# Optimization experiments

Measured on AMD Instinct MI355X. Metric: run time of the kernel, lower is better.

The kernel has to match this reference:

```python
import jax, jax.numpy as jnp
import numpy as np

DIM = 1024
N_HIDDEN = 64
NUM_HEADS = 16
B, S = 4, 1024
# original torch code: scale = sqrt(n_hidden // num_heads) = sqrt(64 // 16) = 2.0
SCALE = float(np.sqrt(N_HIDDEN // NUM_HEADS))


def setup_inputs() -> dict:
    key = jax.random.key(0)
    ks = jax.random.split(key, 10)
    lim = 1.0 / np.sqrt(DIM)          # nn.Linear default init range
    lim_o = 1.0 / np.sqrt(N_HIDDEN * NUM_HEADS)
    u = lambda k, shape, l: jax.random.uniform(k, shape, jnp.float32, -l, l)
    x = jax.random.normal(ks[0], (B, S, DIM), jnp.float32)
    attn_mask = jax.random.randint(ks[1], (B, S, S), 0, 2).astype(jnp.int32)
    # stacked per-head projection weights: [H, dim, n_hidden]
    Wq = u(ks[2], (NUM_HEADS, DIM, N_HIDDEN), lim)
    bq = u(ks[3], (NUM_HEADS, N_HIDDEN), lim)
    Wk = u(ks[4], (NUM_HEADS, DIM, N_HIDDEN), lim)
    bk = u(ks[5], (NUM_HEADS, N_HIDDEN), lim)
    Wv = u(ks[6], (NUM_HEADS, DIM, N_HIDDEN), lim)
    bv = u(ks[7], (NUM_HEADS, N_HIDDEN), lim)
    Wo = u(ks[8], (NUM_HEADS * N_HIDDEN, DIM), lim_o)
    bo = u(ks[9], (DIM,), lim_o)
    return {"x": x, "attn_mask": attn_mask, "Wq": Wq, "bq": bq,
            "Wk": Wk, "bk": bk, "Wv": Wv, "bv": bv, "Wo": Wo, "bo": bo}


def reference(x, attn_mask, Wq, bq, Wk, bk, Wv, bv, Wo, bo):
    # batched QKV across all heads (replaces the per-head Python loop)
    Q = jnp.einsum('bsd,hde->bhse', x, Wq) + bq[None, :, None, :]
    K = jnp.einsum('bsd,hde->bhse', x, Wk) + bk[None, :, None, :]
    V = jnp.einsum('bsd,hde->bhse', x, Wv) + bv[None, :, None, :]
    scores = jnp.einsum('bhse,bhte->bhst', Q, K) / SCALE
    alpha = jax.nn.softmax(scores, axis=-1)
    # faithful to original: zero out masked entries AFTER softmax, no renorm
    alpha = jnp.where(attn_mask[:, None, :, :] == 0, 0.0, alpha)  # [B,H,S,S]
    out = jnp.einsum('bhst,bhte->bhse', alpha, V)                 # [B,H,S,E]
    # torch.cat over heads on last dim == reshape to [B,S,H*E] in head order
    concat = out.transpose(0, 2, 1, 3).reshape(B, S, NUM_HEADS * N_HIDDEN)
    attn_output = concat @ Wo + bo                                # [B,S,dim]
    return attn_output, alpha
```

## Files before the change

kernel.cpp:

```cpp
#include <hip/hip_runtime.h>
#include <stdint.h>

#define S_LEN 1024
#define DIM   1024
#define NHID  64
#define NHEAD 16
#define NB    4

typedef __bf16 bf16x8 __attribute__((ext_vector_type(8)));
typedef float  f32x4  __attribute__((ext_vector_type(4)));
typedef unsigned short u16;

#if defined(__has_builtin)
#if __has_builtin(__builtin_amdgcn_global_load_lds)
#define HAS_GLD 1
#endif
#endif

#ifdef HAS_GLD
#define GLD16(gsrc, ldst)                                                    \
  __builtin_amdgcn_global_load_lds(                                         \
      (const __attribute__((address_space(1))) unsigned int*)(gsrc),        \
      (__attribute__((address_space(3))) unsigned int*)(ldst), 16, 0, 0)
#endif

__device__ __forceinline__ u16 f2b(float f) {
  unsigned u = __float_as_uint(f);
  u += 0x7FFFu + ((u >> 16) & 1u);
  return (u16)(u >> 16);
}

__device__ __forceinline__ f32x4 mfma16(bf16x8 a, bf16x8 b, f32x4 c) {
  return __builtin_amdgcn_mfma_f32_16x16x32_bf16(a, b, c, 0, 0, 0);
}

__global__ __launch_bounds__(256) void k_cvt_x(const float* __restrict__ x,
                                               u16* __restrict__ xb) {
  int i = blockIdx.x * 256 + threadIdx.x;
  float4 v = ((const float4*)x)[i];
  ushort4 o;
  o.x = f2b(v.x); o.y = f2b(v.y); o.z = f2b(v.z); o.w = f2b(v.w);
  ((ushort4*)xb)[i] = o;
}

__global__ __launch_bounds__(256) void k_maskbits(const int* __restrict__ mask,
                                                  uint32_t* __restrict__ bits) {
  int w = blockIdx.x * 256 + threadIdx.x;
  const int4* mp = (const int4*)mask + (size_t)w * 8;
  uint32_t v = 0;
#pragma unroll
  for (int i = 0; i < 8; ++i) {
    int4 m = mp[i];
    v |= (m.x != 0 ? 1u : 0u) << (i * 4 + 0);
    v |= (m.y != 0 ? 1u : 0u) << (i * 4 + 1);
    v |= (m.z != 0 ? 1u : 0u) << (i * 4 + 2);
    v |= (m.w != 0 ? 1u : 0u) << (i * 4 + 3);
  }
  bits[w] = v;
}

__global__ __launch_bounds__(256) void k_transpose(const float* __restrict__ in,
                                                   u16* __restrict__ out,
                                                   int R, int C) {
  const float* ip = in + (size_t)blockIdx.x * R * C;
  u16* op = out + (size_t)blockIdx.x * R * C;
  __shared__ float tile[32][65];
  int r0 = blockIdx.y * 32, c0 = blockIdx.z * 64;
  int t = threadIdx.x;
  {
    int col = t & 63, rr = t >> 6;
#pragma unroll
    for (int p = 0; p < 8; ++p) {
      int r = p * 4 + rr;
      tile[r][col] = ip[(size_t)(r0 + r) * C + c0 + col];
    }
  }
  __syncthreads();
  {
    int d = t & 31, er = t >> 5;
#pragma unroll
    for (int p = 0; p < 8; ++p) {
      int e = p * 8 + er;
      op[(size_t)(c0 + e) * R + r0 + d] = f2b(tile[d][e]);
    }
  }
}

__global__ __launch_bounds__(256) void k_qkv(const u16* __restrict__ xb,
                                             const u16* __restrict__ Wtb,
                                             const float* __restrict__ bq,
                                             const float* __restrict__ bk,
                                             const float* __restrict__ bv,
                                             u16* __restrict__ Qb,
                                             u16* __restrict__ Kb,
                                             u16* __restrict__ Vtb) {
  __shared__ __align__(16) char lds[32768];
  int t = threadIdx.x, w = t >> 6, lane = t & 63;
  int l15 = lane & 15, l4 = lane >> 4;
  int m0 = blockIdx.x * 128, n0 = blockIdx.y * 128, sel = blockIdx.z;
  const u16* Wh = Wtb + (size_t)sel * (NHEAD * NHID * DIM);
  int wr = w >> 1, wc = w & 1;

  f32x4 acc[4][4];
  const f32x4 fz = {0.f, 0.f, 0.f, 0.f};
#pragma unroll
  for (int i = 0; i < 4; ++i)
#pragma unroll
    for (int j = 0; j < 4; ++j) acc[i][j] = fz;

  for (int kk = 0; kk < 16; ++kk) {
    int k0 = kk * 64;
#ifdef HAS_GLD
#pragma unroll
    for (int c = 0; c < 4; ++c) {
      int idx = c * 256 + t, r = idx >> 3, cb = idx & 7;
      int sc_ = cb ^ (r & 7);
      GLD16(xb + (size_t)(m0 + r) * DIM + k0 + sc_ * 8,
            lds + (c * 256 + w * 64) * 16);
    }
#pragma unroll
    for (int c = 0; c < 4; ++c) {
      int idx = c * 256 + t, r = idx >> 3, cb = idx & 7;
      int sc_ = cb ^ (r & 7);
      GLD16(Wh + (size_t)(n0 + r) * DIM + k0 + sc_ * 8,
            lds + 16384 + (c * 256 + w * 64) * 16);
    }
#else
#pragma unroll
    for (int c = 0; c < 4; ++c) {
      int idx = c * 256 + t, r = idx >> 3, cb = idx & 7;
      int4 v = *(const int4*)(xb + (size_t)(m0 + r) * DIM + k0 + cb * 8);
      *(int4*)(lds + r * 128 + ((cb * 16) ^ ((r & 7) << 4))) = v;
    }
#pragma unroll
    for (int c = 0; c < 4; ++c) {
      int idx = c * 256 + t, r = idx >> 3, cb = idx & 7;
      int4 v = *(const int4*)(Wh + (size_t)(n0 + r) * DIM + k0 + cb * 8);
      *(int4*)(lds + 16384 + r * 128 + ((cb * 16) ^ ((r & 7) << 4))) = v;
    }
#endif
    __syncthreads();
    bf16x8 a[4][2], bb[4][2];
#pragma unroll
    for (int mf = 0; mf < 4; ++mf)
#pragma unroll
      for (int kc = 0; kc < 2; ++kc) {
        int row = wr * 64 + mf * 16 + l15;
        int kb = kc * 64 + l4 * 16;
        a[mf][kc] = *(const bf16x8*)(lds + row * 128 + (kb ^ ((row & 7) << 4)));
      }
#pragma unroll
    for (int nf = 0; nf < 4; ++nf)
#pragma unroll
      for (int kc = 0; kc < 2; ++kc) {
        int row = wc * 64 + nf * 16 + l15;
        int kb = kc * 64 + l4 * 16;
        bb[nf][kc] = *(const bf16x8*)(lds + 16384 + row * 128 + (kb ^ ((row & 7) << 4)));
      }
#pragma unroll
    for (int kc = 0; kc < 2; ++kc)
#pragma unroll
      for (int mf = 0; mf < 4; ++mf)
#pragma unroll
        for (int nf = 0; nf < 4; ++nf)
          acc[mf][nf] = mfma16(a[mf][kc], bb[nf][kc], acc[mf][nf]);
    __syncthreads();
  }

  const float* bias = (sel == 0) ? bq : (sel == 1) ? bk : bv;
  float postScale = (sel == 0) ? 0.5f : 1.0f;
#pragma unroll
  for (int nf = 0; nf < 4; ++nf) {
    int n = n0 + wc * 64 + nf * 16 + l15;
    int h = n >> 6, e = n & 63;
    float bv_ = bias[n];
#pragma unroll
    for (int mf = 0; mf < 4; ++mf) {
      int mrow0 = m0 + wr * 64 + mf * 16 + l4 * 4;
      int b_ = mrow0 >> 10, s0 = mrow0 & 1023;
      if (sel == 2) {
        ushort4 pk;
        pk.x = f2b(acc[mf][nf][0] + bv_);
        pk.y = f2b(acc[mf][nf][1] + bv_);
        pk.z = f2b(acc[mf][nf][2] + bv_);
        pk.w = f2b(acc[mf][nf][3] + bv_);
        *(ushort4*)(Vtb + ((size_t)(b_ * NHEAD + h) * NHID + e) * S_LEN + s0) = pk;
      } else {
        u16* dst = (sel == 0) ? Qb : Kb;
#pragma unroll
        for (int j = 0; j < 4; ++j)
          dst[((size_t)(b_ * NHEAD + h) * S_LEN + s0 + j) * NHID + e] =
              f2b((acc[mf][nf][j] + bv_) * postScale);
      }
    }
  }
}

__global__ __launch_bounds__(256) void k_attn(const u16* __restrict__ Qb,
                                              const u16* __restrict__ Kb,
                                              const u16* __restrict__ Vtb,
                                              const uint32_t* __restrict__ mbitsG,
                                              float* __restrict__ alphaOut,
                                              u16* __restrict__ Ob) {
  __shared__ __align__(16) char smem[33024];
  float* redS = (float*)(smem + 32768);
  int t = threadIdx.x, w = t >> 6, lane = t & 63;
  int l15 = lane & 15, l4 = lane >> 4;
  int q0 = blockIdx.x * 16;
  int bh = blockIdx.y, b = bh >> 4, hh = bh & 15;
  const u16* Qh = Qb + (size_t)bh * S_LEN * NHID;
  const u16* Kh = Kb + (size_t)bh * S_LEN * NHID;
  const u16* Vh = Vtb + (size_t)bh * NHID * S_LEN;
  int kbase = w * 256;

  const uint32_t* mrow = mbitsG + ((size_t)b * S_LEN + q0 + l15) * 32 + w * 8;
  uint4 mw0 = *(const uint4*)(mrow);
  uint4 mw1 = *(const uint4*)(mrow + 4);

  bf16x8 aq[2];
#pragma unroll
  for (int ec = 0; ec < 2; ++ec)
    aq[ec] = *(const bf16x8*)(Qh + (size_t)(q0 + l15) * NHID + ec * 32 + l4 * 8);

  const f32x4 fz = {0.f, 0.f, 0.f, 0.f};

  float s0 = 0.f, s1 = 0.f, s2 = 0.f, s3 = 0.f;
#pragma unroll
  for (int kf = 0; kf < 16; ++kf) {
    int key = kbase + kf * 16 + l15;
    bf16x8 kb0 = *(const bf16x8*)(Kh + (size_t)key * NHID + l4 * 8);
    bf16x8 kb1 = *(const bf16x8*)(Kh + (size_t)key * NHID + 32 + l4 * 8);
    f32x4 sct = fz;
    sct = mfma16(kb0, aq[0], sct);
    sct = mfma16(kb1, aq[1], sct);
    float e0 = __expf(sct[0]);
    float e1 = __expf(sct[1]);
    float e2 = __expf(sct[2]);
    float e3 = __expf(sct[3]);
    s0 += e0; s1 += e1; s2 += e2; s3 += e3;
    uint32_t mword;
    switch (kf >> 1) {
      case 0: mword = mw0.x; break;
      case 1: mword = mw0.y; break;
      case 2: mword = mw0.z; break;
      case 3: mword = mw0.w; break;
      case 4: mword = mw1.x; break;
      case 5: mword = mw1.y; break;
      case 6: mword = mw1.z; break;
      default: mword = mw1.w; break;
    }
    int bbase = ((kf & 1) << 4) + l4 * 4;
    uint32_t am01 = (((mword >> (bbase + 0)) & 1u) ? 0x0000FFFFu : 0u) |
                    (((mword >> (bbase + 1)) & 1u) ? 0xFFFF0000u : 0u);
    uint32_t am23 = (((mword >> (bbase + 2)) & 1u) ? 0x0000FFFFu : 0u) |
                    (((mword >> (bbase + 3)) & 1u) ? 0xFFFF0000u : 0u);
    uint2 pk;
    pk.x = ((uint32_t)f2b(e0) | ((uint32_t)f2b(e1) << 16)) & am01;
    pk.y = ((uint32_t)f2b(e2) | ((uint32_t)f2b(e3) << 16)) & am23;
    *(uint2*)(smem + l15 * 2048 +
              (((kbase + kf * 16 + l4 * 4) * 2) ^ ((l15 & 7) << 4))) = pk;
  }
  float ls = (s0 + s1) + (s2 + s3);
  ls += __shfl_xor(ls, 16);
  ls += __shfl_xor(ls, 32);
  if (lane < 16) redS[w * 16 + l15] = ls;
  __syncthreads();

  float* abW = alphaOut + (size_t)bh * S_LEN * S_LEN;
  f32x4 o[4];
#pragma unroll
  for (int ef = 0; ef < 4; ++ef) o[ef] = fz;

  auto rw = [&](int rr) {
    int r = w * 4 + rr;
    float invr = 1.f / (redS[r] + redS[16 + r] + redS[32 + r] + redS[48 + r]);
    float* dst = abW + (size_t)(q0 + r) * S_LEN;
#pragma unroll
    for (int seg = 0; seg < 4; ++seg) {
      int raw = seg * 512 + lane * 8;
      int boff = raw ^ ((r & 7) << 4);
      uint2 pk = *(const uint2*)(smem + r * 2048 + boff);
      f32x4 av;
      av[0] = __uint_as_float(pk.x << 16) * invr;
      av[1] = __uint_as_float(pk.x & 0xFFFF0000u) * invr;
      av[2] = __uint_as_float(pk.y << 16) * invr;
      av[3] = __uint_as_float(pk.y & 0xFFFF0000u) * invr;
      __builtin_nontemporal_store(av, (f32x4*)(dst + (raw >> 1)));
    }
  };
  auto pvc = [&](int c) {
#pragma unroll
    for (int kc2 = 0; kc2 < 2; ++kc2) {
      bf16x8 pa = *(const bf16x8*)(smem + l15 * 2048 +
          ((((kbase + c * 64 + kc2 * 32) * 2) + l4 * 16) ^ ((l15 & 7) << 4)));
#pragma unroll
      for (int ef = 0; ef < 4; ++ef) {
        int e = ef * 16 + l15;
        bf16x8 vb = *(const bf16x8*)(Vh + (size_t)e * S_LEN + kbase + c * 64 +
                                     kc2 * 32 + l4 * 8);
        o[ef] = mfma16(pa, vb, o[ef]);
      }
    }
  };

  rw(0); pvc(0);
  rw(1); pvc(1);
  rw(2); pvc(2);
  rw(3); pvc(3);

  __syncthreads();
  float* redO = (float*)smem;
#pragma unroll
  for (int ef = 0; ef < 4; ++ef)
#pragma unroll
    for (int j = 0; j < 4; ++j)
      redO[w * 1024 + (l4 * 4 + j) * 64 + ef * 16 + l15] = o[ef][j];
  __syncthreads();
  {
    int e = t & 63, r4 = t >> 6;
#pragma unroll
    for (int p = 0; p < 4; ++p) {
      int r = p * 4 + r4;
      float invr = 1.f / (redS[r] + redS[16 + r] + redS[32 + r] + redS[48 + r]);
      float s4 = redO[r * 64 + e] + redO[1024 + r * 64 + e] +
                 redO[2048 + r * 64 + e] + redO[3072 + r * 64 + e];
      Ob[(size_t)(b * S_LEN + q0 + r) * DIM + hh * NHID + e] = f2b(s4 * invr);
    }
  }
}

__global__ __launch_bounds__(256) void k_oproj(const u16* __restrict__ Ob,
                                               const u16* __restrict__ Wotb,
                                               const float* __restrict__ bo,
                                               float* __restrict__ out) {
  __shared__ __align__(16) char lds[32768];
  int t = threadIdx.x, w = t >> 6, lane = t & 63;
  int l15 = lane & 15, l4 = lane >> 4;
  int m0 = blockIdx.x * 128, n0 = blockIdx.y * 128;
  int wr = w >> 1, wc = w & 1;
  f32x4 acc[4][4];
  const f32x4 fz = {0.f, 0.f, 0.f, 0.f};
#pragma unroll
  for (int i = 0; i < 4; ++i)
#pragma unroll
    for (int j = 0; j < 4; ++j) acc[i][j] = fz;

  for (int kk = 0; kk < 16; ++kk) {
    int k0 = kk * 64;
#ifdef HAS_GLD
#pragma unroll
    for (int c = 0; c < 4; ++c) {
      int idx = c * 256 + t, r = idx >> 3, cb = idx & 7;
      int sc_ = cb ^ (r & 7);
      GLD16(Ob + (size_t)(m0 + r) * DIM + k0 + sc_ * 8,
            lds + (c * 256 + w * 64) * 16);
    }
#pragma unroll
    for (int c = 0; c < 4; ++c) {
      int idx = c * 256 + t, r = idx >> 3, cb = idx & 7;
      int sc_ = cb ^ (r & 7);
      GLD16(Wotb + (size_t)(n0 + r) * DIM + k0 + sc_ * 8,
            lds + 16384 + (c * 256 + w * 64) * 16);
    }
#else
#pragma unroll
    for (int c = 0; c < 4; ++c) {
      int idx = c * 256 + t, r = idx >> 3, cb = idx & 7;
      int4 v = *(const int4*)(Ob + (size_t)(m0 + r) * DIM + k0 + cb * 8);
      *(int4*)(lds + r * 128 + ((cb * 16) ^ ((r & 7) << 4))) = v;
    }
#pragma unroll
    for (int c = 0; c < 4; ++c) {
      int idx = c * 256 + t, r = idx >> 3, cb = idx & 7;
      int4 v = *(const int4*)(Wotb + (size_t)(n0 + r) * DIM + k0 + cb * 8);
      *(int4*)(lds + 16384 + r * 128 + ((cb * 16) ^ ((r & 7) << 4))) = v;
    }
#endif
    __syncthreads();
    bf16x8 a[4][2], bb[4][2];
#pragma unroll
    for (int mf = 0; mf < 4; ++mf)
#pragma unroll
      for (int kc = 0; kc < 2; ++kc) {
        int row = wr * 64 + mf * 16 + l15;
        int kb = kc * 64 + l4 * 16;
        a[mf][kc] = *(const bf16x8*)(lds + row * 128 + (kb ^ ((row & 7) << 4)));
      }
#pragma unroll
    for (int nf = 0; nf < 4; ++nf)
#pragma unroll
      for (int kc = 0; kc < 2; ++kc) {
        int row = wc * 64 + nf * 16 + l15;
        int kb = kc * 64 + l4 * 16;
        bb[nf][kc] = *(const bf16x8*)(lds + 16384 + row * 128 + (kb ^ ((row & 7) << 4)));
      }
#pragma unroll
    for (int kc = 0; kc < 2; ++kc)
#pragma unroll
      for (int mf = 0; mf < 4; ++mf)
#pragma unroll
        for (int nf = 0; nf < 4; ++nf)
          acc[mf][nf] = mfma16(a[mf][kc], bb[nf][kc], acc[mf][nf]);
    __syncthreads();
  }
#pragma unroll
  for (int nf = 0; nf < 4; ++nf) {
    int n = n0 + wc * 64 + nf * 16 + l15;
    float bv_ = bo[n];
#pragma unroll
    for (int mf = 0; mf < 4; ++mf)
#pragma unroll
      for (int j = 0; j < 4; ++j) {
        int m = m0 + wr * 64 + mf * 16 + l4 * 4 + j;
        out[(size_t)m * DIM + n] = acc[mf][nf][j] + bv_;
      }
  }
}

extern "C" void kernel_launch(void* const* d_in, const int* in_sizes, int n_in,
                              void* d_out, int out_size, void* d_ws, size_t ws_size,
                              hipStream_t stream) {
  const float* x    = (const float*)d_in[0];
  const int*   mask = (const int*)d_in[1];
  const float* Wq   = (const float*)d_in[2];
  const float* bq   = (const float*)d_in[3];
  const float* Wk   = (const float*)d_in[4];
  const float* bk   = (const float*)d_in[5];
  const float* Wv   = (const float*)d_in[6];
  const float* bv   = (const float*)d_in[7];
  const float* Wo   = (const float*)d_in[8];
  const float* bo   = (const float*)d_in[9];
  float* out = (float*)d_out;
  float* alphaOut = out + (size_t)NB * S_LEN * DIM;

  char* ws = (char*)d_ws;
  u16* xb    = (u16*)(ws);
  u16* Wtb   = (u16*)(ws + 8388608);
  u16* Wotb  = (u16*)(ws + 14680064);
  u16* Qb    = (u16*)(ws + 16777216);
  u16* Kb    = (u16*)(ws + 25165824);
  u16* Vtb   = (u16*)(ws + 33554432);
  u16* Ob    = (u16*)(ws + 41943040);
  uint32_t* mbits = (uint32_t*)(ws + 50331648);

  k_maskbits<<<512, 256, 0, stream>>>(mask, mbits);
  k_cvt_x<<<4096, 256, 0, stream>>>(x, xb);
  k_transpose<<<dim3(16, 32, 1), 256, 0, stream>>>(Wq, Wtb,           1024, 64);
  k_transpose<<<dim3(16, 32, 1), 256, 0, stream>>>(Wk, Wtb + 1048576, 1024, 64);
  k_transpose<<<dim3(16, 32, 1), 256, 0, stream>>>(Wv, Wtb + 2097152, 1024, 64);
  k_transpose<<<dim3(1, 32, 16), 256, 0, stream>>>(Wo, Wotb,          1024, 1024);
  k_qkv<<<dim3(32, 8, 3), 256, 0, stream>>>(xb, Wtb, bq, bk, bv, Qb, Kb, Vtb);
  k_attn<<<dim3(64, 64), 256, 0, stream>>>(Qb, Kb, Vtb, mbits, alphaOut, Ob);
  k_oproj<<<dim3(32, 8), 256, 0, stream>>>(Ob, Wotb, bo, out);
}
```

Baseline: 221.8 us.

## Persistent attention blocks and split PV by head-dim across waves

```diff
diff --git a/kernel.cpp b/kernel.cpp
--- a/kernel.cpp
+++ b/kernel.cpp
@@ -206,125 +206,113 @@
   float* redS = (float*)(smem + 32768);
   int t = threadIdx.x, w = t >> 6, lane = t & 63;
   int l15 = lane & 15, l4 = lane >> 4;
-  int q0 = blockIdx.x * 16;
-  int bh = blockIdx.y, b = bh >> 4, hh = bh & 15;
-  const u16* Qh = Qb + (size_t)bh * S_LEN * NHID;
-  const u16* Kh = Kb + (size_t)bh * S_LEN * NHID;
-  const u16* Vh = Vtb + (size_t)bh * NHID * S_LEN;
+  const f32x4 fz = {0.f, 0.f, 0.f, 0.f};
   int kbase = w * 256;
 
-  const uint32_t* mrow = mbitsG + ((size_t)b * S_LEN + q0 + l15) * 32 + w * 8;
-  uint4 mw0 = *(const uint4*)(mrow);
-  uint4 mw1 = *(const uint4*)(mrow + 4);
-
-  bf16x8 aq[2];
-#pragma unroll
-  for (int ec = 0; ec < 2; ++ec)
-    aq[ec] = *(const bf16x8*)(Qh + (size_t)(q0 + l15) * NHID + ec * 32 + l4 * 8);
-
-  const f32x4 fz = {0.f, 0.f, 0.f, 0.f};
-
-  float s0 = 0.f, s1 = 0.f, s2 = 0.f, s3 = 0.f;
-#pragma unroll
-  for (int kf = 0; kf < 16; ++kf) {
-    int key = kbase + kf * 16 + l15;
-    bf16x8 kb0 = *(const bf16x8*)(Kh + (size_t)key * NHID + l4 * 8);
-    bf16x8 kb1 = *(const bf16x8*)(Kh + (size_t)key * NHID + 32 + l4 * 8);
-    f32x4 sct = fz;
-    sct = mfma16(kb0, aq[0], sct);
-    sct = mfma16(kb1, aq[1], sct);
-    float e0 = __expf(sct[0]);
-    float e1 = __expf(sct[1]);
-    float e2 = __expf(sct[2]);
-    float e3 = __expf(sct[3]);
-    s0 += e0; s1 += e1; s2 += e2; s3 += e3;
-    uint32_t mword;
-    switch (kf >> 1) {
-      case 0: mword = mw0.x; break;
-      case 1: mword = mw0.y; break;
-      case 2: mword = mw0.z; break;
-      case 3: mword = mw0.w; break;
-      case 4: mword = mw1.x; break;
-      case 5: mword = mw1.y; break;
-      case 6: mword = mw1.z; break;
-      default: mword = mw1.w; break;
-    }
-    int bbase = ((kf & 1) << 4) + l4 * 4;
-    uint32_t am01 = (((mword >> (bbase + 0)) & 1u) ? 0x0000FFFFu : 0u) |
-                    (((mword >> (bbase + 1)) & 1u) ? 0xFFFF0000u : 0u);
-    uint32_t am23 = (((mword >> (bbase + 2)) & 1u) ? 0x0000FFFFu : 0u) |
-                    (((mword >> (bbase + 3)) & 1u) ? 0xFFFF0000u : 0u);
-    uint2 pk;
-    pk.x = ((uint32_t)f2b(e0) | ((uint32_t)f2b(e1) << 16)) & am01;
-    pk.y = ((uint32_t)f2b(e2) | ((uint32_t)f2b(e3) << 16)) & am23;
-    *(uint2*)(smem + l15 * 2048 +
-              (((kbase + kf * 16 + l4 * 4) * 2) ^ ((l15 & 7) << 4))) = pk;
-  }
-  float ls = (s0 + s1) + (s2 + s3);
-  ls += __shfl_xor(ls, 16);
-  ls += __shfl_xor(ls, 32);
-  if (lane < 16) redS[w * 16 + l15] = ls;
-  __syncthreads();
-
-  float* abW = alphaOut + (size_t)bh * S_LEN * S_LEN;
-  f32x4 o[4];
-#pragma unroll
-  for (int ef = 0; ef < 4; ++ef) o[ef] = fz;
-
-  auto rw = [&](int rr) {
-    int r = w * 4 + rr;
-    float invr = 1.f / (redS[r] + redS[16 + r] + redS[32 + r] + redS[48 + r]);
-    float* dst = abW + (size_t)(q0 + r) * S_LEN;
-#pragma unroll
-    for (int seg = 0; seg < 4; ++seg) {
-      int raw = seg * 512 + lane * 8;
-      int boff = raw ^ ((r & 7) << 4);
-      uint2 pk = *(const uint2*)(smem + r * 2048 + boff);
-      f32x4 av;
-      av[0] = __uint_as_float(pk.x << 16) * invr;
-      av[1] = __uint_as_float(pk.x & 0xFFFF0000u) * invr;
-      av[2] = __uint_as_float(pk.y << 16) * invr;
-      av[3] = __uint_as_float(pk.y & 0xFFFF0000u) * invr;
-      __builtin_nontemporal_store(av, (f32x4*)(dst + (raw >> 1)));
-    }
-  };
-  auto pvc = [&](int c) {
-#pragma unroll
-    for (int kc2 = 0; kc2 < 2; ++kc2) {
-      bf16x8 pa = *(const bf16x8*)(smem + l15 * 2048 +
-          ((((kbase + c * 64 + kc2 * 32) * 2) + l4 * 16) ^ ((l15 & 7) << 4)));
-#pragma unroll
-      for (int ef = 0; ef < 4; ++ef) {
-        int e = ef * 16 + l15;
-        bf16x8 vb = *(const bf16x8*)(Vh + (size_t)e * S_LEN + kbase + c * 64 +
-                                     kc2 * 32 + l4 * 8);
-        o[ef] = mfma16(pa, vb, o[ef]);
-      }
-    }
-  };
-
-  rw(0); pvc(0);
-  rw(1); pvc(1);
-  rw(2); pvc(2);
-  rw(3); pvc(3);
-
-  __syncthreads();
-  float* redO = (float*)smem;
-#pragma unroll
-  for (int ef = 0; ef < 4; ++ef)
-#pragma unroll
-    for (int j = 0; j < 4; ++j)
-      redO[w * 1024 + (l4 * 4 + j) * 64 + ef * 16 + l15] = o[ef][j];
-  __syncthreads();
-  {
-    int e = t & 63, r4 = t >> 6;
-#pragma unroll
-    for (int p = 0; p < 4; ++p) {
-      int r = p * 4 + r4;
+  for (int ii = blockIdx.x; ii < 4096; ii += 1024) {
+    int bh = ii >> 6, q0 = (ii & 63) * 16;
+    int b = bh >> 4, hh = bh & 15;
+    const u16* Qh = Qb + (size_t)bh * S_LEN * NHID;
+    const u16* Kh = Kb + (size_t)bh * S_LEN * NHID;
+    const u16* Vh = Vtb + (size_t)bh * NHID * S_LEN;
+
+    const uint32_t* mrow = mbitsG + ((size_t)b * S_LEN + q0 + l15) * 32 + w * 8;
+    uint4 mw0 = *(const uint4*)(mrow);
+    uint4 mw1 = *(const uint4*)(mrow + 4);
+
+    bf16x8 aq[2];
+#pragma unroll
+    for (int ec = 0; ec < 2; ++ec)
+      aq[ec] = *(const bf16x8*)(Qh + (size_t)(q0 + l15) * NHID + ec * 32 + l4 * 8);
+
+    if (ii != (int)blockIdx.x) __syncthreads();
+
+    float s0 = 0.f, s1 = 0.f, s2 = 0.f, s3 = 0.f;
+#pragma unroll
+    for (int kf = 0; kf < 16; ++kf) {
+      int key = kbase + kf * 16 + l15;
+      bf16x8 kb0 = *(const bf16x8*)(Kh + (size_t)key * NHID + l4 * 8);
+      bf16x8 kb1 = *(const bf16x8*)(Kh + (size_t)key * NHID + 32 + l4 * 8);
+      f32x4 sct = fz;
+      sct = mfma16(kb0, aq[0], sct);
+      sct = mfma16(kb1, aq[1], sct);
+      float e0 = __expf(sct[0]);
+      float e1 = __expf(sct[1]);
+      float e2 = __expf(sct[2]);
+      float e3 = __expf(sct[3]);
+      s0 += e0; s1 += e1; s2 += e2; s3 += e3;
+      uint32_t mword;
+      switch (kf >> 1) {
+        case 0: mword = mw0.x; break;
+        case 1: mword = mw0.y; break;
+        case 2: mword = mw0.z; break;
+        case 3: mword = mw0.w; break;
+        case 4: mword = mw1.x; break;
+        case 5: mword = mw1.y; break;
+        case 6: mword = mw1.z; break;
+        default: mword = mw1.w; break;
+      }
+      int bbase = ((kf & 1) << 4) + l4 * 4;
+      uint32_t am01 = (((mword >> (bbase + 0)) & 1u) ? 0x0000FFFFu : 0u) |
+                      (((mword >> (bbase + 1)) & 1u) ? 0xFFFF0000u : 0u);
+      uint32_t am23 = (((mword >> (bbase + 2)) & 1u) ? 0x0000FFFFu : 0u) |
+                      (((mword >> (bbase + 3)) & 1u) ? 0xFFFF0000u : 0u);
+      uint2 pk;
+      pk.x = ((uint32_t)f2b(e0) | ((uint32_t)f2b(e1) << 16)) & am01;
+      pk.y = ((uint32_t)f2b(e2) | ((uint32_t)f2b(e3) << 16)) & am23;
+      *(uint2*)(smem + l15 * 2048 +
+                (((kbase + kf * 16 + l4 * 4) * 2) ^ ((l15 & 7) << 4))) = pk;
+    }
+    float ls = (s0 + s1) + (s2 + s3);
+    ls += __shfl_xor(ls, 16);
+    ls += __shfl_xor(ls, 32);
+    if (lane < 16) redS[w * 16 + l15] = ls;
+    __syncthreads();
+
+    float* abW = alphaOut + (size_t)bh * S_LEN * S_LEN;
+    f32x4 o = fz;
+
+    auto rw = [&](int rr) {
+      int r = w * 4 + rr;
       float invr = 1.f / (redS[r] + redS[16 + r] + redS[32 + r] + redS[48 + r]);
-      float s4 = redO[r * 64 + e] + redO[1024 + r * 64 + e] +
-                 redO[2048 + r * 64 + e] + redO[3072 + r * 64 + e];
-      Ob[(size_t)(b * S_LEN + q0 + r) * DIM + hh * NHID + e] = f2b(s4 * invr);
+      float* dst = abW + (size_t)(q0 + r) * S_LEN;
+#pragma unroll
+      for (int seg = 0; seg < 4; ++seg) {
+        int raw = seg * 512 + lane * 8;
+        int boff = raw ^ ((r & 7) << 4);
+        uint2 pk = *(const uint2*)(smem + r * 2048 + boff);
+        f32x4 av;
+        av[0] = __uint_as_float(pk.x << 16) * invr;
+        av[1] = __uint_as_float(pk.x & 0xFFFF0000u) * invr;
+        av[2] = __uint_as_float(pk.y << 16) * invr;
+        av[3] = __uint_as_float(pk.y & 0xFFFF0000u) * invr;
+        __builtin_nontemporal_store(av, (f32x4*)(dst + (raw >> 1)));
+      }
+    };
+    int eS = w * 16 + l15;
+    const u16* Ve = Vh + (size_t)eS * S_LEN;
+    auto pv = [&](int c) {
+#pragma unroll
+      for (int c2 = 0; c2 < 4; ++c2) {
+        int kb_ = c * 128 + c2 * 32;
+        bf16x8 pa = *(const bf16x8*)(smem + l15 * 2048 +
+                     (((kb_ + l4 * 8) * 2) ^ ((l15 & 7) << 4)));
+        bf16x8 vb = *(const bf16x8*)(Ve + kb_ + l4 * 8);
+        o = mfma16(pa, vb, o);
+      }
+    };
+
+    rw(0); pv(0); pv(1);
+    rw(1); pv(2); pv(3);
+    rw(2); pv(4); pv(5);
+    rw(3); pv(6); pv(7);
+
+#pragma unroll
+    for (int j = 0; j < 4; ++j) {
+      int r = l4 * 4 + j;
+      float invr = 1.f / (redS[r] + redS[16 + r] + redS[32 + r] + redS[48 + r]);
+      Ob[(size_t)(b * S_LEN + q0 + r) * DIM + hh * NHID + w * 16 + l15] =
+          f2b(o[j] * invr);
     }
   }
 }
@@ -450,6 +438,6 @@
   k_transpose<<<dim3(16, 32, 1), 256, 0, stream>>>(Wv, Wtb + 2097152, 1024, 64);
   k_transpose<<<dim3(1, 32, 16), 256, 0, stream>>>(Wo, Wotb,          1024, 1024);
   k_qkv<<<dim3(32, 8, 3), 256, 0, stream>>>(xb, Wtb, bq, bk, bv, Qb, Kb, Vtb);
-  k_attn<<<dim3(64, 64), 256, 0, stream>>>(Qb, Kb, Vtb, mbits, alphaOut, Ob);
+  k_attn<<<1024, 256, 0, stream>>>(Qb, Kb, Vtb, mbits, alphaOut, Ob);
   k_oproj<<<dim3(32, 8), 256, 0, stream>>>(Ob, Wotb, bo, out);
 }
```

Measured after the change: 242.0 us. 9.1% more time.
